# Kernel optimization log

Hardware: AMD Instinct MI355X
Metric: run time of the kernel (lower is better)

## Reference

```python
import math
import jax, jax.numpy as jnp
import numpy as np
from jax import lax

B, T, D, H = 4, 1024, 1024, 8192
EPS = 1e-6
PLIF_TH = 0.05        # plif_threshold init
SURR_ALPHA = 2.0      # atan surrogate sharpness
SPARSITY = 0.95

@jax.custom_vjp
def spike(v):
    # Heaviside forward, atan surrogate backward (spikingjelly-style)
    return (v > 0).astype(v.dtype)

def _spike_fwd(v):
    return (v > 0).astype(v.dtype), v

def _spike_bwd(v, g):
    return (g * (SURR_ALPHA / 2.0) / (1.0 + (math.pi / 2.0 * SURR_ALPHA * v) ** 2),)

spike.defvjp(_spike_fwd, _spike_bwd)

def rmsnorm(x, w):
    return x * lax.rsqrt(jnp.mean(x * x, axis=-1, keepdims=True) + EPS) * w

def setup_inputs() -> dict:
    key = jax.random.key(0)
    ks = jax.random.split(key, 12)
    std = 0.02
    return {
        "x": jax.random.normal(ks[0], (B, T, D), jnp.float32),
        "ln1_w": jnp.ones((D,), jnp.float32),
        "liq_Wi": jax.random.normal(ks[1], (D, D), jnp.float32) * std,
        "liq_Wr": jax.random.normal(ks[2], (D, D), jnp.float32) * std,
        "liq_b": jnp.zeros((D,), jnp.float32),
        "liq_tau": 0.5 + jax.random.uniform(ks[3], (D,), jnp.float32),  # positive time constants ('hasani' init)
        "plif_tau": jnp.full((1,), 2.5, jnp.float32),                   # plif_tau_init=2.5
        "syn_w": jax.random.normal(ks[4], (D, D), jnp.float32) * std,
        "gate_w": jax.random.normal(ks[5], (D, D), jnp.float32) * 0.01,
        "gate_b": jnp.zeros((D,), jnp.float32),
        "ln2_w": jnp.ones((D,), jnp.float32),
        "ffn_wg": jax.random.normal(ks[6], (H, D), jnp.float32) * std,
        "ffn_wu": jax.random.normal(ks[7], (H, D), jnp.float32) * std,
        "ffn_wd": jax.random.normal(ks[8], (D, H), jnp.float32) * (std / math.sqrt(2.0)),
        "syn_mask": jax.random.uniform(ks[9], (D, D), jnp.float32) < (1.0 - SPARSITY),
    }

def _forward(x, ln1_w, liq_Wi, liq_Wr, liq_b, liq_tau, plif_tau,
             syn_w, gate_w, gate_b, ln2_w, ffn_wg, ffn_wu, ffn_wd, syn_mask):
    a = rmsnorm(x, ln1_w)                                   # (B,T,D)
    # LiquidCell: ODE-style leaky recurrence, h_t = h*e^{-1/tau} + (1-e^{-1/tau})*tanh(Wi x + Wr h + b)
    decay = jnp.exp(-1.0 / liq_tau)                         # (D,)
    def liq_step(h, xt):
        f = jnp.tanh(xt @ liq_Wi.T + h @ liq_Wr.T + liq_b)
        h2 = h * decay + (1.0 - decay) * f
        return h2, h2
    _, hs = lax.scan(liq_step, jnp.zeros((B, D), x.dtype), jnp.swapaxes(a, 0, 1))
    h = jnp.swapaxes(hs, 0, 1)                              # (B,T,D)
    # PLIFCell.forward_seq: v += (h_t - v)/tau; spike; subtract reset
    inv_tau = 1.0 / plif_tau[0]
    def plif_step(v, ht):
        v = v + (ht - v) * inv_tau
        s = spike(v - PLIF_TH)
        return v - s * PLIF_TH, s
    _, ss = lax.scan(plif_step, jnp.zeros((B, D), x.dtype), jnp.swapaxes(h, 0, 1))
    s = jnp.swapaxes(ss, 0, 1)                              # (B,T,D) binary spikes
    w_eff = syn_w * syn_mask.astype(syn_w.dtype)
    syn_out = s @ w_eff.T
    gated = syn_out * jax.nn.sigmoid(s @ gate_w.T + gate_b)
    x = x + gated
    y = rmsnorm(x, ln2_w)
    ffn = (jax.nn.silu(y @ ffn_wg.T) * (y @ ffn_wu.T)) @ ffn_wd.T
    return x + ffn

def reference(x, ln1_w, liq_Wi, liq_Wr, liq_b, liq_tau, plif_tau,
              syn_w, gate_w, gate_b, ln2_w, ffn_wg, ffn_wu, ffn_wd, syn_mask):
    return _forward(x, ln1_w, liq_Wi, liq_Wr, liq_b, liq_tau, plif_tau,
                    syn_w, gate_w, gate_b, ln2_w, ffn_wg, ffn_wu, ffn_wd, syn_mask)
```

## Files before the change

### kernel.cpp

```cpp
#include <hip/hip_runtime.h>
#include <math.h>


#define Bsz 4
#define Tsz 1024
#define Dsz 1024
#define Hsz 8192

typedef __attribute__((ext_vector_type(8))) short short8;
typedef __attribute__((ext_vector_type(4))) float floatx4_t;


__device__ __forceinline__ unsigned short f2bf(float f) {
  union { float f; unsigned u; } c; c.f = f;
  unsigned x = c.u;
  unsigned r = (x + 0x7FFFu + ((x >> 16) & 1u)) >> 16;
  return (unsigned short)r;
}

__device__ __forceinline__ void gll16(const void* gsrc, void* ldst) {
  __builtin_amdgcn_global_load_lds(
      (const __attribute__((address_space(1))) unsigned int*)gsrc,
      (__attribute__((address_space(3))) unsigned int*)ldst,
      16, 0, 0);
}


__global__ void zero_u64_k(unsigned long long* p, int n) {
  int i = blockIdx.x * 256 + threadIdx.x;
  if (i < n) p[i] = 0ull;
}


template<int BF16OUT>
__global__ __launch_bounds__(256)
void rmsnorm_k(const float* __restrict__ X, const float* __restrict__ w,
               void* __restrict__ out) {
  const long row = blockIdx.x;
  const float* x = X + row * Dsz;
  float4 v = ((const float4*)x)[threadIdx.x];
  float ss = v.x * v.x + v.y * v.y + v.z * v.z + v.w * v.w;
#pragma unroll
  for (int off = 32; off > 0; off >>= 1) ss += __shfl_down(ss, off);
  __shared__ float red[4];
  if ((threadIdx.x & 63) == 0) red[threadIdx.x >> 6] = ss;
  __syncthreads();
  float tot = red[0] + red[1] + red[2] + red[3];
  float scale = 1.0f / sqrtf(tot * (1.0f / Dsz) + 1e-6f);
  float4 wv = ((const float4*)w)[threadIdx.x];
  float o0 = v.x * scale * wv.x, o1 = v.y * scale * wv.y;
  float o2 = v.z * scale * wv.z, o3 = v.w * scale * wv.w;
  if (BF16OUT) {
    ushort4 o; o.x = f2bf(o0); o.y = f2bf(o1); o.z = f2bf(o2); o.w = f2bf(o3);
    ((ushort4*)out)[row * 256 + threadIdx.x] = o;
  } else {
    float4 o; o.x = o0; o.y = o1; o.z = o2; o.w = o3;
    ((float4*)out)[row * 256 + threadIdx.x] = o;
  }
}


__global__ __launch_bounds__(320)
void liquid_plif_k(const float* __restrict__ x,
                   const float* __restrict__ ln1_w,
                   const float* __restrict__ Wi,
                   const float* __restrict__ liq_b,
                   const float* __restrict__ Wr,
                   const float* __restrict__ liq_tau,
                   const float* __restrict__ plif_tau,
                   unsigned long long* __restrict__ Hex,
                   unsigned long long* __restrict__ Utag,
                   unsigned short* __restrict__ Sout,
                   const float* __restrict__ ffn_wg, unsigned short* wg_bf,
                   const float* __restrict__ ffn_wu, unsigned short* wu_bf,
                   const float* __restrict__ ffn_wd, unsigned short* wd_bf,
                   const float* __restrict__ gate_w, unsigned short* gw_bf,
                   const float* __restrict__ syn_w,  const void* mask,
                   unsigned short* weff_bf) {
  const int tid = threadIdx.x;

  __shared__ float h_lds[1024];
  __shared__ __align__(16) float red[2][4][8][4];
  __shared__ int flags[2][4];
  __shared__ float red4w[4];
  __shared__ int s_mode;

  if (tid < 8) ((int*)flags)[tid] = 0;
  __syncthreads();

  if (blockIdx.x < 128) {
    const int blk = blockIdx.x;
    const int b = blk >> 5;
    const int base = (blk & 31) * 32;

    if (tid < 256) {
      const int l = tid & 63, w = tid >> 6;
      const int rg = tid & 7;
      const int ck = tid >> 3;
      const int win = 256 * w;

      float4 wr[4][8];
#pragma unroll
      for (int r = 0; r < 4; ++r) {
        const float* wrow = Wr + (long)(base + rg * 4 + r) * Dsz + ck * 32;
#pragma unroll
        for (int qq = 0; qq < 8; ++qq) {
          int q = (qq + ck) & 7;
          wr[r][qq] = *(const float4*)(wrow + q * 4);
        }
      }

      for (int t = 1; t <= Tsz; ++t) {
        const unsigned want = (unsigned)(t - 1);
        const unsigned long long* src =
            Hex + (((long)((t - 1) & 1) * Bsz + b) << 10) + win;
        unsigned long long a0, a1, a2, a3;
        for (;;) {
          a0 = __hip_atomic_load(src + l,       __ATOMIC_RELAXED, __HIP_MEMORY_SCOPE_AGENT);
          a1 = __hip_atomic_load(src + l + 64,  __ATOMIC_RELAXED, __HIP_MEMORY_SCOPE_AGENT);
          a2 = __hip_atomic_load(src + l + 128, __ATOMIC_RELAXED, __HIP_MEMORY_SCOPE_AGENT);
          a3 = __hip_atomic_load(src + l + 192, __ATOMIC_RELAXED, __HIP_MEMORY_SCOPE_AGENT);
          int ok = ((unsigned)(a0 >> 32) == want) & ((unsigned)(a1 >> 32) == want) &
                   ((unsigned)(a2 >> 32) == want) & ((unsigned)(a3 >> 32) == want);
          if (__all(ok)) break;
        }
        h_lds[win + l]       = __uint_as_float((unsigned)a0);
        h_lds[win + l + 64]  = __uint_as_float((unsigned)a1);
        h_lds[win + l + 128] = __uint_as_float((unsigned)a2);
        h_lds[win + l + 192] = __uint_as_float((unsigned)a3);

        float acc0 = 0.f, acc1 = 0.f, acc2 = 0.f, acc3 = 0.f;
        const float* hch = &h_lds[ck * 32];
#pragma unroll
        for (int qq = 0; qq < 8; ++qq) {
          const int q = (qq + ck) & 7;
          float4 hv = *(const float4*)(hch + q * 4);
          acc0 += wr[0][qq].x * hv.x + wr[0][qq].y * hv.y + wr[0][qq].z * hv.z + wr[0][qq].w * hv.w;
          acc1 += wr[1][qq].x * hv.x + wr[1][qq].y * hv.y + wr[1][qq].z * hv.z + wr[1][qq].w * hv.w;
          acc2 += wr[2][qq].x * hv.x + wr[2][qq].y * hv.y + wr[2][qq].z * hv.z + wr[2][qq].w * hv.w;
          acc3 += wr[3][qq].x * hv.x + wr[3][qq].y * hv.y + wr[3][qq].z * hv.z + wr[3][qq].w * hv.w;
        }
        acc0 += __shfl_xor(acc0, 8); acc0 += __shfl_xor(acc0, 16); acc0 += __shfl_xor(acc0, 32);
        acc1 += __shfl_xor(acc1, 8); acc1 += __shfl_xor(acc1, 16); acc1 += __shfl_xor(acc1, 32);
        acc2 += __shfl_xor(acc2, 8); acc2 += __shfl_xor(acc2, 16); acc2 += __shfl_xor(acc2, 32);
        acc3 += __shfl_xor(acc3, 8); acc3 += __shfl_xor(acc3, 16); acc3 += __shfl_xor(acc3, 32);
        if ((l & 56) == 0) {
          float4 rv; rv.x = acc0; rv.y = acc1; rv.z = acc2; rv.w = acc3;
          *(float4*)&red[t & 1][w][rg][0] = rv;
        }
        asm volatile("s_waitcnt lgkmcnt(0)" ::: "memory");
        if (l == 0)
          __hip_atomic_store(&flags[t & 1][w], t, __ATOMIC_RELEASE,
                             __HIP_MEMORY_SCOPE_WORKGROUP);
      }
    } else {
      const int r = tid - 256;
      float hstate = 0.f, vstate = 0.f, dec = 0.f, omdec = 0.f, itau = 0.f;
      if (r < 32) {
        float tau = liq_tau[base + r];
        dec = expf(-1.0f / tau);
        omdec = 1.0f - dec;
        itau = 1.0f / plif_tau[0];
      }
      for (int t = 1; t <= Tsz; ++t) {
        float uval = 0.f;
        if (r < 32) {
          const unsigned long long* up =
              Utag + ((long)b * Tsz + (t - 1)) * Dsz + base + r;
          unsigned long long uv;
          do {
            uv = __hip_atomic_load(up, __ATOMIC_RELAXED, __HIP_MEMORY_SCOPE_AGENT);
          } while ((unsigned)(uv >> 32) != (unsigned)t);
          uval = __uint_as_float((unsigned)uv);
        }
        const int p = t & 1;
        for (;;) {
          int f0 = __hip_atomic_load(&flags[p][0], __ATOMIC_ACQUIRE, __HIP_MEMORY_SCOPE_WORKGROUP);
          int f1 = __hip_atomic_load(&flags[p][1], __ATOMIC_ACQUIRE, __HIP_MEMORY_SCOPE_WORKGROUP);
          int f2 = __hip_atomic_load(&flags[p][2], __ATOMIC_ACQUIRE, __HIP_MEMORY_SCOPE_WORKGROUP);
          int f3 = __hip_atomic_load(&flags[p][3], __ATOMIC_ACQUIRE, __HIP_MEMORY_SCOPE_WORKGROUP);
          if ((f0 == t) & (f1 == t) & (f2 == t) & (f3 == t)) break;
        }
        if (r < 32) {
          const int r2 = r >> 2, jj = r & 3;
          float sum = red[p][0][r2][jj] + red[p][1][r2][jj] +
                      red[p][2][r2][jj] + red[p][3][r2][jj];
          float z = sum + uval;
          float ex = __expf(2.0f * z);
          float f = 1.0f - 2.0f * __builtin_amdgcn_rcpf(ex + 1.0f);
          hstate = hstate * dec + omdec * f;
          vstate += (hstate - vstate) * itau;
          float sp = ((vstate - 0.05f) > 0.f) ? 1.f : 0.f;
          vstate -= sp * 0.05f;
          const long pidx = (((long)p * Bsz + b) << 10) + base + r;
          unsigned long long pv =
              (((unsigned long long)(unsigned)t) << 32) |
              (unsigned long long)__float_as_uint(hstate);
          __hip_atomic_store(&Hex[pidx], pv, __ATOMIC_RELAXED,
                             __HIP_MEMORY_SCOPE_AGENT);
          Sout[((long)b * Tsz + (t - 1)) * Dsz + base + r] =
              (sp > 0.f) ? (unsigned short)0x3F80 : (unsigned short)0;
        }
      }
    }
  } else {
    const int blk2 = blockIdx.x - 128;
    const int b = blk2 >> 5;
    const int base = (blk2 & 31) * 32;

    const int l = tid & 63, w = tid >> 6;
    const int rg = tid & 7;
    const int ck = tid >> 3;
    float4 wi[4][8];
    if (tid < 256) {
#pragma unroll
      for (int r = 0; r < 4; ++r) {
        const float* wrow = Wi + (long)(base + rg * 4 + r) * Dsz + ck * 32;
#pragma unroll
        for (int qq = 0; qq < 8; ++qq) {
          int q = (qq + ck) & 7;
          wi[r][qq] = *(const float4*)(wrow + q * 4);
        }
      }
    }
    float4 w4 = (tid < 256) ? ((const float4*)ln1_w)[tid] : float4{0, 0, 0, 0};
    float lb = 0.f;
    if (tid >= 256 && (tid - 256) < 32) lb = liq_b[base + (tid - 256)];

    for (int t = 1; t <= Tsz; ++t) {
      float4 xv = {0, 0, 0, 0};
      if (tid < 256) {
        xv = ((const float4*)(x + ((long)b * Tsz + (t - 1)) * Dsz))[tid];
        float ss = xv.x * xv.x + xv.y * xv.y + xv.z * xv.z + xv.w * xv.w;
#pragma unroll
        for (int off = 32; off > 0; off >>= 1) ss += __shfl_down(ss, off);
        if (l == 0) red4w[w] = ss;
      }
      __syncthreads();
      if (tid < 256) {
        float tot = red4w[0] + red4w[1] + red4w[2] + red4w[3];
        float scale = 1.0f / sqrtf(tot * (1.0f / Dsz) + 1e-6f);
        float4 av;
        av.x = xv.x * scale * w4.x; av.y = xv.y * scale * w4.y;
        av.z = xv.z * scale * w4.z; av.w = xv.w * scale * w4.w;
        ((float4*)h_lds)[tid] = av;
      }
      __syncthreads();
      if (tid < 256) {
        float acc0 = 0.f, acc1 = 0.f, acc2 = 0.f, acc3 = 0.f;
        const float* hch = &h_lds[ck * 32];
#pragma unroll
        for (int qq = 0; qq < 8; ++qq) {
          const int q = (qq + ck) & 7;
          float4 hv = *(const float4*)(hch + q * 4);
          acc0 += wi[0][qq].x * hv.x + wi[0][qq].y * hv.y + wi[0][qq].z * hv.z + wi[0][qq].w * hv.w;
          acc1 += wi[1][qq].x * hv.x + wi[1][qq].y * hv.y + wi[1][qq].z * hv.z + wi[1][qq].w * hv.w;
          acc2 += wi[2][qq].x * hv.x + wi[2][qq].y * hv.y + wi[2][qq].z * hv.z + wi[2][qq].w * hv.w;
          acc3 += wi[3][qq].x * hv.x + wi[3][qq].y * hv.y + wi[3][qq].z * hv.z + wi[3][qq].w * hv.w;
        }
        acc0 += __shfl_xor(acc0, 8); acc0 += __shfl_xor(acc0, 16); acc0 += __shfl_xor(acc0, 32);
        acc1 += __shfl_xor(acc1, 8); acc1 += __shfl_xor(acc1, 16); acc1 += __shfl_xor(acc1, 32);
        acc2 += __shfl_xor(acc2, 8); acc2 += __shfl_xor(acc2, 16); acc2 += __shfl_xor(acc2, 32);
        acc3 += __shfl_xor(acc3, 8); acc3 += __shfl_xor(acc3, 16); acc3 += __shfl_xor(acc3, 32);
        if ((l & 56) == 0) {
          float4 rv; rv.x = acc0; rv.y = acc1; rv.z = acc2; rv.w = acc3;
          *(float4*)&red[0][w][rg][0] = rv;
        }
      }
      __syncthreads();
      if (tid >= 256) {
        const int r = tid - 256;
        if (r < 32) {
          const int r2 = r >> 2, jj = r & 3;
          float sum = red[0][0][r2][jj] + red[0][1][r2][jj] +
                      red[0][2][r2][jj] + red[0][3][r2][jj] + lb;
          unsigned long long pv =
              (((unsigned long long)(unsigned)t) << 32) |
              (unsigned long long)__float_as_uint(sum);
          __hip_atomic_store(&Utag[((long)b * Tsz + (t - 1)) * Dsz + base + r],
                             pv, __ATOMIC_RELAXED, __HIP_MEMORY_SCOPE_AGENT);
        }
      }
      __syncthreads();
    }

    if (tid == 0) {
      int md = 0;
      const unsigned* m = (const unsigned*)mask;
      for (int i = 0; i < 256; ++i) {
        unsigned wd = m[i];
        if (wd == 0x3F800000u) { md = 2; break; }
        if (wd > 1u) md = 1;
      }
      s_mode = md;
    }
    __syncthreads();
    const int md = s_mode;
    const long gtid = (long)blk2 * 320 + tid;
    const long gstr = 128 * 320;
    const int n4big = Hsz * Dsz / 4;
    for (long i = gtid; i < n4big; i += gstr) {
      float4 v = ((const float4*)ffn_wg)[i];
      ushort4 o; o.x = f2bf(v.x); o.y = f2bf(v.y); o.z = f2bf(v.z); o.w = f2bf(v.w);
      ((ushort4*)wg_bf)[i] = o;
      v = ((const float4*)ffn_wu)[i];
      o.x = f2bf(v.x); o.y = f2bf(v.y); o.z = f2bf(v.z); o.w = f2bf(v.w);
      ((ushort4*)wu_bf)[i] = o;
      v = ((const float4*)ffn_wd)[i];
      o.x = f2bf(v.x); o.y = f2bf(v.y); o.z = f2bf(v.z); o.w = f2bf(v.w);
      ((ushort4*)wd_bf)[i] = o;
    }
    const int n4g = Dsz * Dsz / 4;
    for (long i = gtid; i < n4g; i += gstr) {
      float4 v = ((const float4*)gate_w)[i];
      ushort4 o; o.x = f2bf(v.x); o.y = f2bf(v.y); o.z = f2bf(v.z); o.w = f2bf(v.w);
      ((ushort4*)gw_bf)[i] = o;
    }
    const int nw = Dsz * Dsz;
    for (long i = gtid; i < nw; i += gstr) {
      bool on;
      if (md == 1)      on = ((const unsigned char*)mask)[i] != 0;
      else if (md == 2) on = ((const float*)mask)[i] != 0.f;
      else              on = ((const int*)mask)[i] != 0;
      weff_bf[i] = on ? f2bf(syn_w[i]) : (unsigned short)0;
    }
  }
}


template<int NB, int EPI>
__global__ __launch_bounds__(256)
void gemm_bt(const unsigned short* __restrict__ A,
             const unsigned short* __restrict__ B0,
             const unsigned short* __restrict__ B1,
             const float* __restrict__ aux0, const float* __restrict__ aux1,
             void* __restrict__ outp, int M, int N, int K) {
  __shared__ unsigned short sA[128 * 32];
  __shared__ unsigned short sB[2 * 128 * 32];
  const int tid = threadIdx.x;
  const int w = tid >> 6, l = tid & 63;
  const int wm = w & 1, wn = w >> 1;
  const int bm = blockIdx.x, bn = blockIdx.y;

  floatx4_t acc[NB][4][4];
#pragma unroll
  for (int j = 0; j < NB; ++j)
#pragma unroll
    for (int m = 0; m < 4; ++m)
#pragma unroll
      for (int n = 0; n < 4; ++n) acc[j][m][n] = (floatx4_t)(0.f);

  const int rA = bm * 128 + 16 * w + (l >> 2);
  const int rB = bn * 128 + 16 * w + (l >> 2);
  const int kl = (l & 3) * 8;
  const unsigned short* gA = A + (long)rA * K + kl;
  const unsigned short* gB0 = B0 + (long)rB * K + kl;
  const unsigned short* gB1 = nullptr;
  if constexpr (NB > 1) gB1 = B1 + (long)rB * K + kl;
  unsigned short* lA = &sA[(16 * w) * 32];
  unsigned short* lB = &sB[(16 * w) * 32];

  for (int k0 = 0; k0 < K; k0 += 32) {
    gll16(gA + k0,              lA);
    gll16(gA + k0 + 64 * K,     lA + 64 * 32);
    gll16(gB0 + k0,             lB);
    gll16(gB0 + k0 + 64 * K,    lB + 64 * 32);
    if constexpr (NB > 1) {
      gll16(gB1 + k0,           lB + 128 * 32);
      gll16(gB1 + k0 + 64 * K,  lB + 192 * 32);
    }
    __syncthreads();
    short8 af[4];
#pragma unroll
    for (int m = 0; m < 4; ++m)
      af[m] = *(const short8*)&sA[(wm * 64 + m * 16 + (l & 15)) * 32 + (l >> 4) * 8];
#pragma unroll
    for (int j = 0; j < NB; ++j) {
#pragma unroll
      for (int n = 0; n < 4; ++n) {
        short8 bf = *(const short8*)&sB[j * 128 * 32 +
                        (wn * 64 + n * 16 + (l & 15)) * 32 + (l >> 4) * 8];
#pragma unroll
        for (int m = 0; m < 4; ++m)
          acc[j][m][n] = __builtin_amdgcn_mfma_f32_16x16x32_bf16(
              af[m], bf, acc[j][m][n], 0, 0, 0);
      }
    }
    __syncthreads();
  }

  const int colBase = bn * 128 + wn * 64;
  const int rowBase = bm * 128 + wm * 64;
#pragma unroll
  for (int m = 0; m < 4; ++m) {
#pragma unroll
    for (int n = 0; n < 4; ++n) {
      const int col = colBase + n * 16 + (l & 15);
#pragma unroll
      for (int j = 0; j < 4; ++j) {
        const int row = rowBase + m * 16 + (l >> 4) * 4 + j;
        const long idx = (long)row * N + col;
        float v0 = acc[0][m][n][j];
        if constexpr (EPI == 1) {
          float gsum = acc[NB - 1][m][n][j] + aux1[col];
          float sg = 1.f / (1.f + __expf(-gsum));
          ((float*)outp)[idx] = aux0[idx] + v0 * sg;
        } else if constexpr (EPI == 2) {
          float sil = v0 / (1.f + __expf(-v0));
          ((unsigned short*)outp)[idx] = f2bf(sil * acc[NB - 1][m][n][j]);
        } else {
          ((float*)outp)[idx] = aux0[idx] + v0;
        }
      }
    }
  }
}


extern "C" void kernel_launch(void* const* d_in, const int* in_sizes, int n_in,
                              void* d_out, int out_size, void* d_ws, size_t ws_size,
                              hipStream_t stream) {
  (void)in_sizes; (void)n_in; (void)out_size; (void)ws_size;

  const float* x        = (const float*)d_in[0];
  const float* ln1_w    = (const float*)d_in[1];
  const float* liq_Wi   = (const float*)d_in[2];
  const float* liq_Wr   = (const float*)d_in[3];
  const float* liq_b    = (const float*)d_in[4];
  const float* liq_tau  = (const float*)d_in[5];
  const float* plif_tau = (const float*)d_in[6];
  const float* syn_w    = (const float*)d_in[7];
  const float* gate_w   = (const float*)d_in[8];
  const float* gate_b   = (const float*)d_in[9];
  const float* ln2_w    = (const float*)d_in[10];
  const float* ffn_wg   = (const float*)d_in[11];
  const float* ffn_wu   = (const float*)d_in[12];
  const float* ffn_wd   = (const float*)d_in[13];
  const void*  mask     = d_in[14];

  char* ws = (char*)d_ws;
  const size_t MB = 1024ull * 1024ull;
  unsigned short* wg_bf   = (unsigned short*)(ws + 0 * MB);
  unsigned short* wu_bf   = (unsigned short*)(ws + 16 * MB);
  unsigned short* wd_bf   = (unsigned short*)(ws + 32 * MB);
  unsigned short* weff_bf = (unsigned short*)(ws + 48 * MB);
  unsigned short* gw_bf   = (unsigned short*)(ws + 50 * MB);
  float*          x2_f    = (float*)         (ws + 52 * MB);
  unsigned short* s_bf    = (unsigned short*)(ws + 68 * MB);
  unsigned short* y_bf    = (unsigned short*)(ws + 76 * MB);
  unsigned short* ff_bf   = (unsigned short*)(ws + 84 * MB);
  unsigned long long* Utag= (unsigned long long*)(ws + 84 * MB);
  unsigned long long* hex = (unsigned long long*)(ws + 148 * MB);
  float*          out_f   = (float*)d_out;

  const int M = Bsz * Tsz;

  zero_u64_k<<<32, 256, 0, stream>>>(hex, 2 * Bsz * Dsz);

  liquid_plif_k<<<256, 320, 0, stream>>>(
      x, ln1_w, liq_Wi, liq_b, liq_Wr, liq_tau, plif_tau, hex, Utag, s_bf,
      ffn_wg, wg_bf, ffn_wu, wu_bf, ffn_wd, wd_bf, gate_w, gw_bf,
      syn_w, mask, weff_bf);

  gemm_bt<2, 1><<<dim3(M / 128, Dsz / 128), 256, 0, stream>>>(
      s_bf, weff_bf, gw_bf, x, gate_b, x2_f, M, Dsz, Dsz);

  rmsnorm_k<1><<<M, 256, 0, stream>>>(x2_f, ln2_w, y_bf);

  gemm_bt<2, 2><<<dim3(M / 128, Hsz / 128), 256, 0, stream>>>(
      y_bf, wg_bf, wu_bf, nullptr, nullptr, ff_bf, M, Hsz, Dsz);

  gemm_bt<1, 3><<<dim3(M / 128, Dsz / 128), 256, 0, stream>>>(
      ff_bf, wd_bf, nullptr, x2_f, nullptr, out_f, M, Dsz, Hsz);
}
```

Baseline: 2.213 ms.

## Overlap synapse GEMM and RMSNorm with recurrence via per-timestep progress flags

The 128 helper blocks of the recurrence kernel now convert the gate and masked synapse weights first and publish a completion flag. For most time chunks they then wait on per-block spike progress counters and compute the gated synapse GEMM, residual add and RMSNorm for 32-row tiles while the scan is still running. Only the last time chunks go through the separate GEMM and RMSNorm launches, and the zeroing kernel is folded into the main kernel. The overlap aims to hide synapse GEMM time behind the serial recurrence, at the cost of spin-waits, unstaged global-memory MFMA operand loads and a delay to the FFN weight conversion.

Result: slower. 4.192 ms (+89.4%).

```diff
diff --git a/kernel.cpp b/kernel.cpp
--- a/kernel.cpp
+++ b/kernel.cpp
@@ -6,6 +6,8 @@
 #define Tsz 1024
 #define Dsz 1024
 #define Hsz 8192
+#define JCUT 24
+#define MAGICC 0x5EEDC0DEu
 
 typedef __attribute__((ext_vector_type(8))) short short8;
 typedef __attribute__((ext_vector_type(4))) float floatx4_t;
@@ -18,6 +20,11 @@
   return (unsigned short)r;
 }
 
+__device__ __forceinline__ unsigned long long pack4bf(float4 v) {
+  unsigned long long a = f2bf(v.x), b = f2bf(v.y), c = f2bf(v.z), d = f2bf(v.w);
+  return a | (b << 16) | (c << 32) | (d << 48);
+}
+
 __device__ __forceinline__ void gll16(const void* gsrc, void* ldst) {
   __builtin_amdgcn_global_load_lds(
       (const __attribute__((address_space(1))) unsigned int*)gsrc,
@@ -26,17 +33,10 @@
 }
 
 
-__global__ void zero_u64_k(unsigned long long* p, int n) {
-  int i = blockIdx.x * 256 + threadIdx.x;
-  if (i < n) p[i] = 0ull;
-}
-
-
-template<int BF16OUT>
 __global__ __launch_bounds__(256)
 void rmsnorm_k(const float* __restrict__ X, const float* __restrict__ w,
-               void* __restrict__ out) {
-  const long row = blockIdx.x;
+               unsigned short* __restrict__ out, int rowBase) {
+  const long row = (long)blockIdx.y * 1024 + rowBase + blockIdx.x;
   const float* x = X + row * Dsz;
   float4 v = ((const float4*)x)[threadIdx.x];
   float ss = v.x * v.x + v.y * v.y + v.z * v.z + v.w * v.w;
@@ -48,15 +48,10 @@
   float tot = red[0] + red[1] + red[2] + red[3];
   float scale = 1.0f / sqrtf(tot * (1.0f / Dsz) + 1e-6f);
   float4 wv = ((const float4*)w)[threadIdx.x];
-  float o0 = v.x * scale * wv.x, o1 = v.y * scale * wv.y;
-  float o2 = v.z * scale * wv.z, o3 = v.w * scale * wv.w;
-  if (BF16OUT) {
-    ushort4 o; o.x = f2bf(o0); o.y = f2bf(o1); o.z = f2bf(o2); o.w = f2bf(o3);
-    ((ushort4*)out)[row * 256 + threadIdx.x] = o;
-  } else {
-    float4 o; o.x = o0; o.y = o1; o.z = o2; o.w = o3;
-    ((float4*)out)[row * 256 + threadIdx.x] = o;
-  }
+  ushort4 o;
+  o.x = f2bf(v.x * scale * wv.x); o.y = f2bf(v.y * scale * wv.y);
+  o.z = f2bf(v.z * scale * wv.z); o.w = f2bf(v.w * scale * wv.w);
+  ((ushort4*)out)[row * 256 + threadIdx.x] = o;
 }
 
 
@@ -68,9 +63,15 @@
                    const float* __restrict__ Wr,
                    const float* __restrict__ liq_tau,
                    const float* __restrict__ plif_tau,
+                   const float* __restrict__ gate_b,
+                   const float* __restrict__ ln2_w,
                    unsigned long long* __restrict__ Hex,
                    unsigned long long* __restrict__ Utag,
                    unsigned short* __restrict__ Sout,
+                   unsigned* __restrict__ SProg,
+                   unsigned* __restrict__ ConvD,
+                   float* __restrict__ x2_f,
+                   unsigned short* __restrict__ y_bf,
                    const float* __restrict__ ffn_wg, unsigned short* wg_bf,
                    const float* __restrict__ ffn_wu, unsigned short* wu_bf,
                    const float* __restrict__ ffn_wd, unsigned short* wd_bf,
@@ -83,15 +84,24 @@
   __shared__ __align__(16) float red[2][4][8][4];
   __shared__ int flags[2][4];
   __shared__ float red4w[4];
+  __shared__ float ssq_l[4][32];
   __shared__ int s_mode;
 
   if (tid < 8) ((int*)flags)[tid] = 0;
-  __syncthreads();
 
   if (blockIdx.x < 128) {
     const int blk = blockIdx.x;
     const int b = blk >> 5;
     const int base = (blk & 31) * 32;
+
+    if (tid < 64) {
+      const long zp = (((long)(tid >> 5) * Bsz + b) << 10) + base + (tid & 31);
+      __hip_atomic_store(&Hex[zp], 0ull, __ATOMIC_RELAXED, __HIP_MEMORY_SCOPE_AGENT);
+    }
+    if (tid == 64)
+      __hip_atomic_store(&SProg[(b << 5) + (blk & 31)], 0u,
+                         __ATOMIC_RELAXED, __HIP_MEMORY_SCOPE_AGENT);
+    __syncthreads();
 
     if (tid < 256) {
       const int l = tid & 63, w = tid >> 6;
@@ -198,8 +208,12 @@
               (unsigned long long)__float_as_uint(hstate);
           __hip_atomic_store(&Hex[pidx], pv, __ATOMIC_RELAXED,
                              __HIP_MEMORY_SCOPE_AGENT);
-          Sout[((long)b * Tsz + (t - 1)) * Dsz + base + r] =
-              (sp > 0.f) ? (unsigned short)0x3F80 : (unsigned short)0;
+          __hip_atomic_store(&Sout[((long)b * Tsz + (t - 1)) * Dsz + base + r],
+                             (unsigned short)((sp > 0.f) ? 0x3F80 : 0),
+                             __ATOMIC_RELAXED, __HIP_MEMORY_SCOPE_AGENT);
+          if (r == 0)
+            __hip_atomic_store(&SProg[(b << 5) + (blk & 31)], (unsigned)t,
+                               __ATOMIC_RELEASE, __HIP_MEMORY_SCOPE_AGENT);
         }
       }
     }
@@ -207,8 +221,51 @@
     const int blk2 = blockIdx.x - 128;
     const int b = blk2 >> 5;
     const int base = (blk2 & 31) * 32;
-
     const int l = tid & 63, w = tid >> 6;
+
+    if (tid == 0) {
+      int md = 0;
+      const unsigned* m = (const unsigned*)mask;
+      for (int i = 0; i < 256; ++i) {
+        unsigned wd = m[i];
+        if (wd == 0x3F800000u) { md = 2; break; }
+        if (wd > 1u) md = 1;
+      }
+      s_mode = md;
+    }
+    __syncthreads();
+    {
+      const int md = s_mode;
+      const long gt = (long)blk2 * 320 + tid, gs = 128 * 320;
+      const int n4 = Dsz * Dsz / 4;
+      for (long i = gt; i < n4; i += gs) {
+        float4 g = ((const float4*)gate_w)[i];
+        __hip_atomic_store((unsigned long long*)gw_bf + i, pack4bf(g),
+                           __ATOMIC_RELAXED, __HIP_MEMORY_SCOPE_AGENT);
+        float4 s = ((const float4*)syn_w)[i];
+        bool on0, on1, on2, on3;
+        if (md == 1) {
+          const unsigned char* mp = (const unsigned char*)mask + i * 4;
+          on0 = mp[0]; on1 = mp[1]; on2 = mp[2]; on3 = mp[3];
+        } else if (md == 2) {
+          const float* mp = (const float*)mask + i * 4;
+          on0 = mp[0] != 0.f; on1 = mp[1] != 0.f; on2 = mp[2] != 0.f; on3 = mp[3] != 0.f;
+        } else {
+          const int* mp = (const int*)mask + i * 4;
+          on0 = mp[0]; on1 = mp[1]; on2 = mp[2]; on3 = mp[3];
+        }
+        float4 sv;
+        sv.x = on0 ? s.x : 0.f; sv.y = on1 ? s.y : 0.f;
+        sv.z = on2 ? s.z : 0.f; sv.w = on3 ? s.w : 0.f;
+        __hip_atomic_store((unsigned long long*)weff_bf + i, pack4bf(sv),
+                           __ATOMIC_RELAXED, __HIP_MEMORY_SCOPE_AGENT);
+      }
+    }
+    __syncthreads();
+    if (tid == 0)
+      __hip_atomic_store(&ConvD[blk2], MAGICC, __ATOMIC_RELEASE,
+                         __HIP_MEMORY_SCOPE_AGENT);
+
     const int rg = tid & 7;
     const int ck = tid >> 3;
     float4 wi[4][8];
@@ -284,45 +341,117 @@
       __syncthreads();
     }
 
-    if (tid == 0) {
-      int md = 0;
-      const unsigned* m = (const unsigned*)mask;
-      for (int i = 0; i < 256; ++i) {
-        unsigned wd = m[i];
-        if (wd == 0x3F800000u) { md = 2; break; }
-        if (wd > 1u) md = 1;
-      }
-      s_mode = md;
-    }
-    __syncthreads();
-    const int md = s_mode;
-    const long gtid = (long)blk2 * 320 + tid;
-    const long gstr = 128 * 320;
-    const int n4big = Hsz * Dsz / 4;
-    for (long i = gtid; i < n4big; i += gstr) {
-      float4 v = ((const float4*)ffn_wg)[i];
-      ushort4 o; o.x = f2bf(v.x); o.y = f2bf(v.y); o.z = f2bf(v.z); o.w = f2bf(v.w);
-      ((ushort4*)wg_bf)[i] = o;
-      v = ((const float4*)ffn_wu)[i];
-      o.x = f2bf(v.x); o.y = f2bf(v.y); o.z = f2bf(v.z); o.w = f2bf(v.w);
-      ((ushort4*)wu_bf)[i] = o;
-      v = ((const float4*)ffn_wd)[i];
-      o.x = f2bf(v.x); o.y = f2bf(v.y); o.z = f2bf(v.z); o.w = f2bf(v.w);
-      ((ushort4*)wd_bf)[i] = o;
-    }
-    const int n4g = Dsz * Dsz / 4;
-    for (long i = gtid; i < n4g; i += gstr) {
-      float4 v = ((const float4*)gate_w)[i];
-      ushort4 o; o.x = f2bf(v.x); o.y = f2bf(v.y); o.z = f2bf(v.z); o.w = f2bf(v.w);
-      ((ushort4*)gw_bf)[i] = o;
-    }
-    const int nw = Dsz * Dsz;
-    for (long i = gtid; i < nw; i += gstr) {
-      bool on;
-      if (md == 1)      on = ((const unsigned char*)mask)[i] != 0;
-      else if (md == 2) on = ((const float*)mask)[i] != 0.f;
-      else              on = ((const int*)mask)[i] != 0;
-      weff_bf[i] = on ? f2bf(syn_w[i]) : (unsigned short)0;
+    const int j = blk2 & 31;
+    if (j < JCUT) {
+      const unsigned t_hi = (unsigned)(j * 32 + 32);
+      const long r0g = (long)b * 1024 + j * 32;
+
+      for (;;) {
+        unsigned c0 = __hip_atomic_load(&ConvD[l], __ATOMIC_ACQUIRE, __HIP_MEMORY_SCOPE_AGENT);
+        unsigned c1 = __hip_atomic_load(&ConvD[l + 64], __ATOMIC_ACQUIRE, __HIP_MEMORY_SCOPE_AGENT);
+        if (__all((c0 == MAGICC) & (c1 == MAGICC))) break;
+      }
+      for (;;) {
+        unsigned pk = __hip_atomic_load(&SProg[(b << 5) + (l & 31)],
+                                        __ATOMIC_ACQUIRE, __HIP_MEMORY_SCOPE_AGENT);
+        if (__all((pk >= t_hi) & (pk <= (unsigned)Tsz))) break;
+      }
+
+      float ssq8[8] = {0.f, 0.f, 0.f, 0.f, 0.f, 0.f, 0.f, 0.f};
+      if (tid < 256) {
+        const int cw = w * 64;
+#pragma unroll 1
+        for (int bn = 0; bn < 4; ++bn) {
+          const int cbase = bn * 256 + cw;
+          floatx4_t acc[2][2][4];
+#pragma unroll
+          for (int mt = 0; mt < 2; ++mt)
+#pragma unroll
+            for (int m = 0; m < 2; ++m)
+#pragma unroll
+              for (int n = 0; n < 4; ++n) acc[mt][m][n] = (floatx4_t)(0.f);
+          const int fr = (l & 15), fk = (l >> 4) * 8;
+#pragma unroll 2
+          for (int kc = 0; kc < 32; ++kc) {
+            const int ko = kc * 32 + fk;
+            short8 af0 = *(const short8*)&Sout[(r0g + fr) * Dsz + ko];
+            short8 af1 = *(const short8*)&Sout[(r0g + 16 + fr) * Dsz + ko];
+#pragma unroll
+            for (int n = 0; n < 4; ++n) {
+              const long brow = (long)(cbase + n * 16 + fr) * Dsz + ko;
+              short8 bf0 = *(const short8*)&weff_bf[brow];
+              short8 bf1 = *(const short8*)&gw_bf[brow];
+              acc[0][0][n] = __builtin_amdgcn_mfma_f32_16x16x32_bf16(af0, bf0, acc[0][0][n], 0, 0, 0);
+              acc[0][1][n] = __builtin_amdgcn_mfma_f32_16x16x32_bf16(af1, bf0, acc[0][1][n], 0, 0, 0);
+              acc[1][0][n] = __builtin_amdgcn_mfma_f32_16x16x32_bf16(af0, bf1, acc[1][0][n], 0, 0, 0);
+              acc[1][1][n] = __builtin_amdgcn_mfma_f32_16x16x32_bf16(af1, bf1, acc[1][1][n], 0, 0, 0);
+            }
+          }
+#pragma unroll
+          for (int m = 0; m < 2; ++m)
+#pragma unroll
+            for (int n = 0; n < 4; ++n) {
+              const int c = cbase + n * 16 + fr;
+#pragma unroll
+              for (int q = 0; q < 4; ++q) {
+                const int r = m * 16 + (l >> 4) * 4 + q;
+                const long idx = (r0g + r) * Dsz + c;
+                float gsum = acc[1][m][n][q] + gate_b[c];
+                float sg = 1.f / (1.f + __expf(-gsum));
+                float x2v = x[idx] + acc[0][m][n][q] * sg;
+                x2_f[idx] = x2v;
+                ssq8[m * 4 + q] += x2v * x2v;
+              }
+            }
+        }
+#pragma unroll
+        for (int i = 0; i < 8; ++i) {
+          float v = ssq8[i];
+          v += __shfl_xor(v, 1); v += __shfl_xor(v, 2);
+          v += __shfl_xor(v, 4); v += __shfl_xor(v, 8);
+          ssq8[i] = v;
+        }
+        if ((l & 15) == 0) {
+#pragma unroll
+          for (int m = 0; m < 2; ++m)
+#pragma unroll
+            for (int q = 0; q < 4; ++q)
+              ssq_l[w][m * 16 + (l >> 4) * 4 + q] = ssq8[m * 4 + q];
+        }
+      }
+      __syncthreads();
+      if (tid < 256) {
+        const int row = tid >> 3, cg = tid & 7;
+        float tot = ssq_l[0][row] + ssq_l[1][row] + ssq_l[2][row] + ssq_l[3][row];
+        float scale = 1.0f / sqrtf(tot * (1.0f / Dsz) + 1e-6f);
+        const long gr = r0g + row;
+#pragma unroll 4
+        for (int i = 0; i < 32; ++i) {
+          const int c = cg * 128 + i * 4;
+          float4 xv = *(const float4*)&x2_f[gr * Dsz + c];
+          float4 wv = *(const float4*)&ln2_w[c];
+          ushort4 o;
+          o.x = f2bf(xv.x * scale * wv.x); o.y = f2bf(xv.y * scale * wv.y);
+          o.z = f2bf(xv.z * scale * wv.z); o.w = f2bf(xv.w * scale * wv.w);
+          *(ushort4*)&y_bf[gr * Dsz + c] = o;
+        }
+      }
+    }
+
+    {
+      const long gt = (long)blk2 * 320 + tid, gs = 128 * 320;
+      const int n4big = Hsz * Dsz / 4;
+      for (long i = gt; i < n4big; i += gs) {
+        float4 v = ((const float4*)ffn_wg)[i];
+        ushort4 o; o.x = f2bf(v.x); o.y = f2bf(v.y); o.z = f2bf(v.z); o.w = f2bf(v.w);
+        ((ushort4*)wg_bf)[i] = o;
+        v = ((const float4*)ffn_wu)[i];
+        o.x = f2bf(v.x); o.y = f2bf(v.y); o.z = f2bf(v.z); o.w = f2bf(v.w);
+        ((ushort4*)wu_bf)[i] = o;
+        v = ((const float4*)ffn_wd)[i];
+        o.x = f2bf(v.x); o.y = f2bf(v.y); o.z = f2bf(v.z); o.w = f2bf(v.w);
+        ((ushort4*)wd_bf)[i] = o;
+      }
     }
   }
 }
@@ -334,13 +463,15 @@
              const unsigned short* __restrict__ B0,
              const unsigned short* __restrict__ B1,
              const float* __restrict__ aux0, const float* __restrict__ aux1,
-             void* __restrict__ outp, int M, int N, int K) {
+             void* __restrict__ outp, int M, int N, int K,
+             int R, int rowBase) {
   __shared__ unsigned short sA[128 * 32];
   __shared__ unsigned short sB[2 * 128 * 32];
   const int tid = threadIdx.x;
   const int w = tid >> 6, l = tid & 63;
   const int wm = w & 1, wn = w >> 1;
   const int bm = blockIdx.x, bn = blockIdx.y;
+  const int rowStart = (bm / R) * 1024 + rowBase + (bm % R) * 128;
 
   floatx4_t acc[NB][4][4];
 #pragma unroll
@@ -350,7 +481,7 @@
 #pragma unroll
       for (int n = 0; n < 4; ++n) acc[j][m][n] = (floatx4_t)(0.f);
 
-  const int rA = bm * 128 + 16 * w + (l >> 2);
+  const int rA = rowStart + 16 * w + (l >> 2);
   const int rB = bn * 128 + 16 * w + (l >> 2);
   const int kl = (l & 3) * 8;
   const unsigned short* gA = A + (long)rA * K + kl;
@@ -390,7 +521,7 @@
   }
 
   const int colBase = bn * 128 + wn * 64;
-  const int rowBase = bm * 128 + wm * 64;
+  const int rowBase2 = rowStart + wm * 64;
 #pragma unroll
   for (int m = 0; m < 4; ++m) {
 #pragma unroll
@@ -398,7 +529,7 @@
       const int col = colBase + n * 16 + (l & 15);
 #pragma unroll
       for (int j = 0; j < 4; ++j) {
-        const int row = rowBase + m * 16 + (l >> 4) * 4 + j;
+        const int row = rowBase2 + m * 16 + (l >> 4) * 4 + j;
         const long idx = (long)row * N + col;
         float v0 = acc[0][m][n][j];
         if constexpr (EPI == 1) {
@@ -451,25 +582,25 @@
   unsigned short* ff_bf   = (unsigned short*)(ws + 84 * MB);
   unsigned long long* Utag= (unsigned long long*)(ws + 84 * MB);
   unsigned long long* hex = (unsigned long long*)(ws + 148 * MB);
+  unsigned*       SProg   = (unsigned*)(ws + 148 * MB + 65536);
+  unsigned*       ConvD   = (unsigned*)(ws + 148 * MB + 66048);
   float*          out_f   = (float*)d_out;
 
   const int M = Bsz * Tsz;
 
-  zero_u64_k<<<32, 256, 0, stream>>>(hex, 2 * Bsz * Dsz);
-
   liquid_plif_k<<<256, 320, 0, stream>>>(
-      x, ln1_w, liq_Wi, liq_b, liq_Wr, liq_tau, plif_tau, hex, Utag, s_bf,
+      x, ln1_w, liq_Wi, liq_b, liq_Wr, liq_tau, plif_tau, gate_b, ln2_w,
+      hex, Utag, s_bf, SProg, ConvD, x2_f, y_bf,
       ffn_wg, wg_bf, ffn_wu, wu_bf, ffn_wd, wd_bf, gate_w, gw_bf,
       syn_w, mask, weff_bf);
 
-  gemm_bt<2, 1><<<dim3(M / 128, Dsz / 128), 256, 0, stream>>>(
-      s_bf, weff_bf, gw_bf, x, gate_b, x2_f, M, Dsz, Dsz);
-
-  rmsnorm_k<1><<<M, 256, 0, stream>>>(x2_f, ln2_w, y_bf);
+  gemm_bt<2, 1><<<dim3(8, Dsz / 128), 256, 0, stream>>>(
+      s_bf, weff_bf, gw_bf, x, gate_b, x2_f, M, Dsz, Dsz, 2, JCUT * 32);
+  rmsnorm_k<<<dim3(256, 4), 256, 0, stream>>>(x2_f, ln2_w, y_bf, JCUT * 32);
 
   gemm_bt<2, 2><<<dim3(M / 128, Hsz / 128), 256, 0, stream>>>(
-      y_bf, wg_bf, wu_bf, nullptr, nullptr, ff_bf, M, Hsz, Dsz);
+      y_bf, wg_bf, wu_bf, nullptr, nullptr, ff_bf, M, Hsz, Dsz, 8, 0);
 
   gemm_bt<1, 3><<<dim3(M / 128, Dsz / 128), 256, 0, stream>>>(
-      ff_bf, wd_bf, nullptr, x2_f, nullptr, out_f, M, Dsz, Hsz);
+      ff_bf, wd_bf, nullptr, x2_f, nullptr, out_f, M, Dsz, Hsz, 8, 0);
 }
```
